# Kernel optimization log

Measured on AMD Instinct MI355X. Metric: run time of the kernel, lower is better.

## Reference

```python
import jax, jax.numpy as jnp
import numpy as np

B, N, D_IN = 2, 2048, 2048
D_OUT, H, KV = 2048, 32, 8
G = H // KV          # group_size = 4
DH = D_OUT // H      # head dim = 64


def setup_inputs() -> dict:
    key = jax.random.key(0)
    k0, k1, k2, k3, k4, k5 = jax.random.split(key, 6)
    s_in = 1.0 / np.sqrt(D_IN)
    s_out = 1.0 / np.sqrt(D_OUT)
    return {
        "x": jax.random.normal(k0, (B, N, D_IN), dtype=jnp.float32),
        "Wq": jax.random.normal(k1, (D_IN, H * DH), dtype=jnp.float32) * s_in,
        "Wk": jax.random.normal(k2, (D_IN, KV * DH), dtype=jnp.float32) * s_in,
        "Wv": jax.random.normal(k3, (D_IN, KV * DH), dtype=jnp.float32) * s_in,
        "Wo": jax.random.normal(k4, (D_OUT, D_IN), dtype=jnp.float32) * s_out,
        "bo": jax.random.normal(k5, (D_IN,), dtype=jnp.float32) * 0.01,
    }


def gqa_forward(x, Wq, Wk, Wv, Wo, bo):
    b, n, _ = x.shape
    scale = 1.0 / jnp.sqrt(jnp.asarray(DH, x.dtype))
    # projections
    q = (x @ Wq).reshape(b, n, KV, G, DH)   # queries grouped by shared kv head
    k = (x @ Wk).reshape(b, n, KV, DH)
    v = (x @ Wv).reshape(b, n, KV, DH)
    # scores: (B, KV, G, N, N) — equivalent to repeat_interleave of K over groups
    scores = jnp.einsum('bnkgd,bmkd->bkgnm', q, k) * scale
    causal = jnp.triu(jnp.ones((n, n), dtype=bool), k=1)
    scores = jnp.where(causal, -jnp.inf, scores)
    attn = jax.nn.softmax(scores, axis=-1)
    # dropout p=0.0 -> identity
    ctx = jnp.einsum('bkgnm,bmkd->bnkgd', attn, v).reshape(b, n, D_OUT)
    return ctx @ Wo + bo


def reference(x, Wq, Wk, Wv, Wo, bo):
    return gqa_forward(x, Wq, Wk, Wv, Wo, bo)
```

## Files before the change

### kernel.cpp

```cpp
#include <hip/hip_runtime.h>
#include <hip/hip_bf16.h>
#include <cstdint>


#define B_    2
#define N_    2048
#define DIN_  2048
#define H_    32
#define KV_   8
#define DH_   64
#define M_    4096
#define NQKV_ 3072

typedef float f32x4 __attribute__((ext_vector_type(4)));
typedef __bf16 bf16x8 __attribute__((ext_vector_type(8)));
typedef unsigned short u16x8 __attribute__((ext_vector_type(8)));

__device__ __forceinline__ unsigned short f32_to_bf16_bits(float f) {
  unsigned int u = __float_as_uint(f);
  u = (u + 0x7FFFu + ((u >> 16) & 1u)) >> 16;
  return (unsigned short)u;
}

__device__ __forceinline__ void gload_lds16(const void* g, void* l) {
  __builtin_amdgcn_global_load_lds(
      (__attribute__((address_space(1))) void*)(g),
      (__attribute__((address_space(3))) void*)(l), 16, 0, 0);
}

__global__ __launch_bounds__(256) void prep(
    const float* __restrict__ x, const float* __restrict__ Wq,
    const float* __restrict__ Wk, const float* __restrict__ Wv,
    const float* __restrict__ Wo,
    unsigned short* __restrict__ Xb, unsigned short* __restrict__ Wqkv,
    unsigned short* __restrict__ Wot, float qscale) {
  const int task = blockIdx.y, tid = threadIdx.x;
  if (task == 0) {
    size_t base = (size_t)blockIdx.x * 1024;
#pragma unroll
    for (int t = 0; t < 4; ++t) {
      size_t i = base + t * 256 + tid;
      float4 v = ((const float4*)x)[i];
      ushort4 o;
      o.x = f32_to_bf16_bits(v.x);
      o.y = f32_to_bf16_bits(v.y);
      o.z = f32_to_bf16_bits(v.z);
      o.w = f32_to_bf16_bits(v.w);
      ((ushort4*)Xb)[i] = o;
    }
    return;
  }
  const float* src;
  unsigned short* dst;
  int NC, off;
  float scale = 1.0f;
  switch (task) {
    case 1: src = Wq; dst = Wqkv; NC = 2048; off = 0;    scale = qscale; break;
    case 2: src = Wk; dst = Wqkv; NC = 512;  off = 2048; break;
    case 3: src = Wv; dst = Wqkv; NC = 512;  off = 2560; break;
    default: src = Wo; dst = Wot; NC = 2048; off = 0;    break;
  }
  const int nbn = NC >> 6;
  if (blockIdx.x >= 32 * nbn) return;
  const int n0 = (blockIdx.x % nbn) * 64, k0 = (blockIdx.x / nbn) * 64;

  __shared__ float tile[64][68];
  const int tx = tid & 15, ty = tid >> 4;
#pragma unroll
  for (int i = 0; i < 4; ++i) {
    float4 v = *(const float4*)&src[(size_t)(k0 + i * 16 + ty) * NC + n0 + tx * 4];
    *(float4*)&tile[i * 16 + ty][tx * 4] = v;
  }
  __syncthreads();
  const int n = tid >> 2, kc = (tid & 3) * 16;
  unsigned short* drow = dst + (size_t)(off + n0 + n) * 2048 + k0 + kc;
#pragma unroll
  for (int h = 0; h < 2; ++h) {
    u16x8 o;
#pragma unroll
    for (int j = 0; j < 8; ++j)
      o[j] = f32_to_bf16_bits(tile[kc + h * 8 + j][n] * scale);
    *(u16x8*)(drow + h * 8) = o;
  }
}

__global__ __launch_bounds__(256) void transpose_v(
    const unsigned short* __restrict__ QKV, unsigned short* __restrict__ Vtg) {
  __shared__ unsigned short t[64][72];
  int nt = blockIdx.x, bkv = blockIdx.y;
  int b = bkv >> 3, kv = bkv & 7;
  int tid = threadIdx.x;
  int row = tid >> 2, c = (tid & 3) * 16;
  const unsigned short* src =
      QKV + (size_t)(b * N_ + nt * 64 + row) * NQKV_ + 2560 + kv * 64;
  *(u16x8*)&t[row][c]     = *(const u16x8*)(src + c);
  *(u16x8*)&t[row][c + 8] = *(const u16x8*)(src + c + 8);
  __syncthreads();
  int d = tid >> 2;
  unsigned short* dst = Vtg + ((size_t)bkv * 64 + d) * N_ + nt * 64 + c;
  u16x8 o0, o1;
#pragma unroll
  for (int i = 0; i < 8; ++i) { o0[i] = t[c + i][d]; o1[i] = t[c + 8 + i][d]; }
  *(u16x8*)dst = o0;
  *(u16x8*)(dst + 8) = o1;
}

template <int BM, int BN, bool OUT_BF16, bool BIAS>
__global__ __launch_bounds__(512, 2) void gemm256p(
    const unsigned short* __restrict__ A,
    const unsigned short* __restrict__ Bt,
    void* __restrict__ Cv,
    const float* __restrict__ bias,
    int Nn, int K, int nbx) {
  constexpr int AL = BM / 64;
  constexpr int BL = BN / 64;
  constexpr int STL = AL + BL;
  constexpr int RM = BM / 2;
  constexpr int CW = BN / 4;
  constexpr int MI = RM / 16;
  constexpr int NI = CW / 16;
  constexpr int NP = MI / 2;

  __shared__ unsigned short ldsA[2][BM * 64];
  __shared__ unsigned short ldsB[2][BN * 64];

  const int tid = threadIdx.x;
  const int lane = tid & 63;
  const int wave = tid >> 6;
  const int wm = wave >> 2, wn = wave & 3;
  const int l16 = lane & 15, quad = lane >> 4;

  const int nwg = gridDim.x;
  const int orig = blockIdx.x;
  const int bid = (orig & 7) * (nwg >> 3) + (orig >> 3);
  const int m0 = (bid / nbx) * BM, n0 = (bid % nbx) * BN;

  const int T = K >> 6;

  auto stage = [&](int c) {
    const int buf = c & 1;
#pragma unroll
    for (int i = 0; i < AL; ++i) {
      int off = i * 8192 + tid * 16;
      int row = off >> 7;
      int kch = ((off >> 4) & 7) ^ (row & 7);
      gload_lds16(A + (size_t)(m0 + row) * K + c * 64 + kch * 8,
                  (char*)&ldsA[buf][0] + off);
    }
#pragma unroll
    for (int i = 0; i < BL; ++i) {
      int off = i * 8192 + tid * 16;
      int row = off >> 7;
      int kch = ((off >> 4) & 7) ^ (row & 7);
      gload_lds16(Bt + (size_t)(n0 + row) * K + c * 64 + kch * 8,
                  (char*)&ldsB[buf][0] + off);
    }
  };

  const int sw7 = l16 & 7;
  const int cA0 = ((0 * 4 + quad) ^ sw7) * 16;
  const int cA1 = ((1 * 4 + quad) ^ sw7) * 16;
  const int rowA = (wm * RM + l16) * 128;
  const int rowB = (wn * CW + l16) * 128;

  f32x4 acc[MI][NI] = {};

  stage(0);
  stage(1);

  for (int c = 0; c < T; ++c) {
    if (c + 1 < T) {
      if constexpr (STL == 6)      asm volatile("s_waitcnt vmcnt(6)" ::: "memory");
      else if constexpr (STL == 7) asm volatile("s_waitcnt vmcnt(7)" ::: "memory");
      else                         asm volatile("s_waitcnt vmcnt(8)" ::: "memory");
    } else {
      asm volatile("s_waitcnt vmcnt(0)" ::: "memory");
    }
    __builtin_amdgcn_s_barrier();
    asm volatile("" ::: "memory");

    const char* Ar = (const char*)&ldsA[c & 1][0];
    const char* Br = (const char*)&ldsB[c & 1][0];

    bf16x8 b[NI][2];
#pragma unroll
    for (int ni = 0; ni < NI; ++ni) {
      b[ni][0] = *(const bf16x8*)(Br + rowB + ni * 2048 + cA0);
      b[ni][1] = *(const bf16x8*)(Br + rowB + ni * 2048 + cA1);
    }
    bf16x8 ap[2][2][2];
#pragma unroll
    for (int ml = 0; ml < 2; ++ml) {
      ap[0][ml][0] = *(const bf16x8*)(Ar + rowA + ml * 2048 + cA0);
      ap[0][ml][1] = *(const bf16x8*)(Ar + rowA + ml * 2048 + cA1);
    }
    asm volatile("s_waitcnt lgkmcnt(0)" ::: "memory");
    __builtin_amdgcn_sched_barrier(0);

#pragma unroll
    for (int p = 0; p < NP; ++p) {
      if (p < NP - 1) {
        const int nx = (p + 1) & 1;
#pragma unroll
        for (int ml = 0; ml < 2; ++ml) {
          int mi = (p + 1) * 2 + ml;
          ap[nx][ml][0] = *(const bf16x8*)(Ar + rowA + mi * 2048 + cA0);
          ap[nx][ml][1] = *(const bf16x8*)(Ar + rowA + mi * 2048 + cA1);
        }
      }
      __builtin_amdgcn_sched_barrier(0);
      __builtin_amdgcn_s_setprio(1);
#pragma unroll
      for (int ml = 0; ml < 2; ++ml)
#pragma unroll
        for (int ni = 0; ni < NI; ++ni)
#pragma unroll
          for (int ks = 0; ks < 2; ++ks)
            acc[p * 2 + ml][ni] = __builtin_amdgcn_mfma_f32_16x16x32_bf16(
                ap[p & 1][ml][ks], b[ni][ks], acc[p * 2 + ml][ni], 0, 0, 0);
      __builtin_amdgcn_s_setprio(0);
      if (p < NP - 1) {
        asm volatile("s_waitcnt lgkmcnt(0)" ::: "memory");
        __builtin_amdgcn_sched_barrier(0);
      }
    }

    asm volatile("" ::: "memory");
    __builtin_amdgcn_s_barrier();
    asm volatile("" ::: "memory");
    if (c + 2 < T) stage(c + 2);
  }

  unsigned short* Cb = (unsigned short*)Cv;
  float* Cf = (float*)Cv;
#pragma unroll
  for (int mi = 0; mi < MI; ++mi) {
    int rrow = m0 + wm * RM + mi * 16 + quad * 4;
#pragma unroll
    for (int ni = 0; ni < NI; ++ni) {
      int col = n0 + wn * CW + ni * 16 + l16;
      float bv = BIAS ? bias[col] : 0.0f;
#pragma unroll
      for (int r = 0; r < 4; ++r) {
        float v = acc[mi][ni][r] + bv;
        if (OUT_BF16)
          Cb[(size_t)(rrow + r) * Nn + col] = f32_to_bf16_bits(v);
        else
          Cf[(size_t)(rrow + r) * Nn + col] = v;
      }
    }
  }
}

__global__ __launch_bounds__(512, 4) void attn_fwd(
    const unsigned short* __restrict__ QKV,
    const unsigned short* __restrict__ Vtg,
    unsigned short* __restrict__ Ctx) {
  __shared__ unsigned short Ks[2][64 * 64];
  __shared__ unsigned short Vs[2][64 * 64];
  __shared__ unsigned short Ps[2][8][16 * 64];

  const int p = blockIdx.x;
  const int kv = blockIdx.y >> 1, hp = blockIdx.y & 1;
  const int b = blockIdx.z;
  const int tid = threadIdx.x, lane = tid & 63, wave = tid >> 6;
  const int l16 = lane & 15, quad = lane >> 4;
  const int h = kv * 4 + hp * 2 + (wave >> 2);
  const int rstrip = (wave & 3) * 16;
  const size_t baserow = (size_t)b * N_;
  const unsigned short* Kg = QKV + 2048 + kv * 64;
  const unsigned short* Vg = Vtg + (size_t)(b * KV_ + kv) * 64 * N_;
  const unsigned short* Qbase = QKV + baserow * NQKV_ + h * 64;
  const int sw = l16 & 7;

  auto stageKV = [&](int j, int buf) {
    int c = tid;
    int row = c >> 3, off = ((c & 7) ^ (row & 7)) * 8;
    gload_lds16(Kg + (baserow + j * 64 + row) * NQKV_ + off,
                (char*)Ks[buf] + c * 16);
    gload_lds16(Vg + (size_t)row * N_ + j * 64 + off,
                (char*)Vs[buf] + c * 16);
  };

#pragma unroll 1
  for (int phase = 0; phase < 2; ++phase) {
    const int qtile = phase ? p : 31 - p;
    const int q0 = qtile * 64;

    bf16x8 qa[2];
#pragma unroll
    for (int ks = 0; ks < 2; ++ks)
      qa[ks] = *(const bf16x8*)(Qbase +
          (size_t)(q0 + rstrip + l16) * NQKV_ + ks * 32 + quad * 8);

    f32x4 oacc[4] = {};
    float lp[4] = {};

    __syncthreads();
    stageKV(0, 0);

    for (int j = 0; j <= qtile; ++j) {
      __syncthreads();
      const int buf = j & 1;
      if (j < qtile) stageKV(j + 1, buf ^ 1);

      bf16x8 kb[2][4];
#pragma unroll
      for (int ks = 0; ks < 2; ++ks)
#pragma unroll
        for (int ni = 0; ni < 4; ++ni)
          kb[ks][ni] = *(const bf16x8*)&Ks[buf][(ni * 16 + l16) * 64 +
                                               ((ks * 4 + quad) ^ sw) * 8];

      f32x4 sc[4] = {};
      __builtin_amdgcn_s_setprio(1);
#pragma unroll
      for (int ks = 0; ks < 2; ++ks)
#pragma unroll
        for (int ni = 0; ni < 4; ++ni)
          sc[ni] = __builtin_amdgcn_mfma_f32_16x16x32_bf16(
              qa[ks], kb[ks][ni], sc[ni], 0, 0, 0);
      __builtin_amdgcn_s_setprio(0);
      if (j == qtile) {
        const int qrow = q0 + rstrip + quad * 4;
#pragma unroll
        for (int ni = 0; ni < 4; ++ni) {
          int kcol = q0 + ni * 16 + l16;
#pragma unroll
          for (int r = 0; r < 4; ++r)
            if (kcol > qrow + r) sc[ni][r] = -1e30f;
        }
      }
      unsigned short* Pw = &Ps[buf][wave][0];
#pragma unroll
      for (int ni = 0; ni < 4; ++ni) {
        const int cl = ni * 2 + (l16 >> 3);
#pragma unroll
        for (int r = 0; r < 4; ++r) {
          float pe = __builtin_amdgcn_exp2f(sc[ni][r]);
          lp[r] += pe;
          int row = quad * 4 + r;
          Pw[row * 64 + ((cl ^ (row & 7)) * 8) + (l16 & 7)] =
              (unsigned short)(__float_as_uint(pe) >> 16);
        }
      }

      bf16x8 vb[2][4];
#pragma unroll
      for (int ks = 0; ks < 2; ++ks)
#pragma unroll
        for (int di = 0; di < 4; ++di)
          vb[ks][di] = *(const bf16x8*)&Vs[buf][(di * 16 + l16) * 64 +
                                               ((ks * 4 + quad) ^ sw) * 8];
      bf16x8 pa[2];
#pragma unroll
      for (int ks = 0; ks < 2; ++ks)
        pa[ks] = *(const bf16x8*)&Ps[buf][wave][l16 * 64 +
                                               ((ks * 4 + quad) ^ sw) * 8];
      __builtin_amdgcn_s_setprio(1);
#pragma unroll
      for (int ks = 0; ks < 2; ++ks)
#pragma unroll
        for (int di = 0; di < 4; ++di)
          oacc[di] = __builtin_amdgcn_mfma_f32_16x16x32_bf16(
              pa[ks], vb[ks][di], oacc[di], 0, 0, 0);
      __builtin_amdgcn_s_setprio(0);
    }

    float inv[4];
#pragma unroll
    for (int r = 0; r < 4; ++r) {
      float v = lp[r];
#pragma unroll
      for (int off = 1; off < 16; off <<= 1) v += __shfl_xor(v, off);
      inv[r] = 1.0f / v;
    }
#pragma unroll
    for (int di = 0; di < 4; ++di)
#pragma unroll
      for (int r = 0; r < 4; ++r) {
        size_t row = baserow + q0 + rstrip + quad * 4 + r;
        Ctx[row * 2048 + h * 64 + di * 16 + l16] =
            f32_to_bf16_bits(oacc[di][r] * inv[r]);
      }
  }
}

extern "C" void kernel_launch(void* const* d_in, const int* in_sizes, int n_in,
                              void* d_out, int out_size, void* d_ws, size_t ws_size,
                              hipStream_t stream) {
  const float* x  = (const float*)d_in[0];
  const float* Wq = (const float*)d_in[1];
  const float* Wk = (const float*)d_in[2];
  const float* Wv = (const float*)d_in[3];
  const float* Wo = (const float*)d_in[4];
  const float* bo = (const float*)d_in[5];
  float* out = (float*)d_out;

  unsigned short* Xb   = (unsigned short*)d_ws;
  unsigned short* Wqkv = Xb + (size_t)M_ * DIN_;
  unsigned short* QKV  = Wqkv + (size_t)NQKV_ * DIN_;
  unsigned short* Wot  = QKV + (size_t)M_ * NQKV_;
  unsigned short* Ctx  = Xb;
  unsigned short* Vtg  = Wqkv;

  const float kQScale = 0.125f * 1.44269504088896340736f;

  prep<<<dim3(2048, 5), 256, 0, stream>>>(x, Wq, Wk, Wv, Wo, Xb, Wqkv, Wot, kQScale);

  gemm256p<256, 192, true, false><<<dim3(256), 512, 0, stream>>>(
      Xb, Wqkv, QKV, nullptr, NQKV_, DIN_, NQKV_ / 192);

  transpose_v<<<dim3(N_ / 64, B_ * KV_), 256, 0, stream>>>(QKV, Vtg);

  attn_fwd<<<dim3(16, 16, 2), 512, 0, stream>>>(QKV, Vtg, Ctx);

  gemm256p<256, 128, false, true><<<dim3(256), 512, 0, stream>>>(
      Ctx, Wot, out, bo, DIN_, 2048, DIN_ / 128);
}
```

Baseline: 277.9 us.

## Software-pipeline attention loop: overlap QK of next tile with PV of current

Splits K and V staging and restructures the causal attention inner loop into a skewed pipeline. K is prefetched two tiles ahead and V one tile ahead, and each iteration runs PV for tile j alongside QK/softmax for tile j+1, with a prologue and an epilogue around the loop. The aim is to give the scheduler independent MFMA and LDS work to interleave, hiding exp and LDS latency between the two matmuls. The cost is more live registers (score and output accumulators held together) and more complex buffer indexing.

```diff
diff --git a/kernel.cpp b/kernel.cpp
--- a/kernel.cpp
+++ b/kernel.cpp
@@ -273,11 +273,15 @@
   const unsigned short* Qbase = QKV + baserow * NQKV_ + h * 64;
   const int sw = l16 & 7;
 
-  auto stageKV = [&](int j, int buf) {
+  auto stageK = [&](int j, int buf) {
     int c = tid;
     int row = c >> 3, off = ((c & 7) ^ (row & 7)) * 8;
     gload_lds16(Kg + (baserow + j * 64 + row) * NQKV_ + off,
                 (char*)Ks[buf] + c * 16);
+  };
+  auto stageV = [&](int j, int buf) {
+    int c = tid;
+    int row = c >> 3, off = ((c & 7) ^ (row & 7)) * 8;
     gload_lds16(Vg + (size_t)row * N_ + j * 64 + off,
                 (char*)Vs[buf] + c * 16);
   };
@@ -296,22 +300,15 @@
     f32x4 oacc[4] = {};
     float lp[4] = {};
 
-    __syncthreads();
-    stageKV(0, 0);
-
-    for (int j = 0; j <= qtile; ++j) {
-      __syncthreads();
-      const int buf = j & 1;
-      if (j < qtile) stageKV(j + 1, buf ^ 1);
-
+    auto doQK = [&](int jj) {
+      const int kbuf = jj & 1;
       bf16x8 kb[2][4];
 #pragma unroll
       for (int ks = 0; ks < 2; ++ks)
 #pragma unroll
         for (int ni = 0; ni < 4; ++ni)
-          kb[ks][ni] = *(const bf16x8*)&Ks[buf][(ni * 16 + l16) * 64 +
+          kb[ks][ni] = *(const bf16x8*)&Ks[kbuf][(ni * 16 + l16) * 64 +
                                                ((ks * 4 + quad) ^ sw) * 8];
-
       f32x4 sc[4] = {};
       __builtin_amdgcn_s_setprio(1);
 #pragma unroll
@@ -321,7 +318,7 @@
           sc[ni] = __builtin_amdgcn_mfma_f32_16x16x32_bf16(
               qa[ks], kb[ks][ni], sc[ni], 0, 0, 0);
       __builtin_amdgcn_s_setprio(0);
-      if (j == qtile) {
+      if (jj == qtile) {
         const int qrow = q0 + rstrip + quad * 4;
 #pragma unroll
         for (int ni = 0; ni < 4; ++ni) {
@@ -331,7 +328,7 @@
             if (kcol > qrow + r) sc[ni][r] = -1e30f;
         }
       }
-      unsigned short* Pw = &Ps[buf][wave][0];
+      unsigned short* Pw = &Ps[kbuf][wave][0];
 #pragma unroll
       for (int ni = 0; ni < 4; ++ni) {
         const int cl = ni * 2 + (l16 >> 3);
@@ -344,18 +341,21 @@
               (unsigned short)(__float_as_uint(pe) >> 16);
         }
       }
-
+    };
+
+    auto doPV = [&](int jj) {
+      const int vbuf = jj & 1;
       bf16x8 vb[2][4];
 #pragma unroll
       for (int ks = 0; ks < 2; ++ks)
 #pragma unroll
         for (int di = 0; di < 4; ++di)
-          vb[ks][di] = *(const bf16x8*)&Vs[buf][(di * 16 + l16) * 64 +
+          vb[ks][di] = *(const bf16x8*)&Vs[vbuf][(di * 16 + l16) * 64 +
                                                ((ks * 4 + quad) ^ sw) * 8];
       bf16x8 pa[2];
 #pragma unroll
       for (int ks = 0; ks < 2; ++ks)
-        pa[ks] = *(const bf16x8*)&Ps[buf][wave][l16 * 64 +
+        pa[ks] = *(const bf16x8*)&Ps[vbuf][wave][l16 * 64 +
                                                ((ks * 4 + quad) ^ sw) * 8];
       __builtin_amdgcn_s_setprio(1);
 #pragma unroll
@@ -365,7 +365,26 @@
           oacc[di] = __builtin_amdgcn_mfma_f32_16x16x32_bf16(
               pa[ks], vb[ks][di], oacc[di], 0, 0, 0);
       __builtin_amdgcn_s_setprio(0);
-    }
+    };
+
+    __syncthreads();
+    stageK(0, 0);
+    stageV(0, 0);
+    if (qtile >= 1) stageK(1, 1);
+    __syncthreads();
+    doQK(0);
+
+#pragma unroll 1
+    for (int j = 0; j < qtile; ++j) {
+      __syncthreads();
+      if (j + 2 <= qtile) stageK(j + 2, j & 1);
+      stageV(j + 1, (j + 1) & 1);
+      doPV(j);
+      doQK(j + 1);
+    }
+
+    __syncthreads();
+    doPV(qtile);
 
     float inv[4];
 #pragma unroll
```

Result: slower. 283.8 us (+2.1%).
